# Optimization experiments

Hardware: AMD Instinct MI355X
Metric: run time of the kernel (lower is better)

Reference implementation:

```python
import jax, jax.numpy as jnp
import numpy as np

B, L, W = 512, 16, 256


def setup_inputs() -> dict:
    key = jax.random.key(0)
    k = jax.random.split(key, 9)
    f32 = jnp.float32
    # spin configuration in {-1, +1}
    x = jax.random.randint(k[0], (B, L, L), 0, 2).astype(f32) * 2.0 - 1.0
    s = 1.0 / np.sqrt(W)
    W_ih = jax.random.normal(k[1], (3 * W, 2), f32) * s      # GRUCell input weights
    W_hh = jax.random.normal(k[2], (3 * W, W), f32) * s      # GRUCell hidden weights
    b_ih = jax.random.normal(k[3], (3 * W,), f32) * s
    b_hh = jax.random.normal(k[4], (3 * W,), f32) * s
    W_fc = jax.random.normal(k[5], (2, W), f32) * s          # fc1
    b_fc = jax.random.normal(k[6], (2,), f32) * s
    W_hcat = jax.random.normal(k[7], (W, 2 * W), f32) * (1.0 / np.sqrt(2 * W))  # intermediate_h
    W_xcat = jax.random.normal(k[8], (1, 2), f32) * 0.5      # intermediate_x
    return dict(x=x, W_ih=W_ih, W_hh=W_hh, b_ih=b_ih, b_hh=b_hh,
                W_fc=W_fc, b_fc=b_fc, W_hcat=W_hcat, W_xcat=W_xcat)


def _log_prob(x, W_ih, W_hh, b_ih, b_hh, W_fc, b_fc, W_hcat, W_xcat):
    Bsz, Ln, _ = x.shape
    Wd = W_hh.shape[1]
    mask = (1.0 + x) * 0.5                      # (1+x)/2
    Wh_l = W_hcat[:, :Wd]                       # acts on left-neighbor hidden (cat order: [left, up])
    Wh_u = W_hcat[:, Wd:]                       # acts on up-neighbor hidden

    def step(carry, xs):
        x_left, h_left = carry                  # [B], [B,W]
        x_cur, x_up, h_up, m = xs               # [B], [B], [B,W], [B]
        # intermediate_x(stack([x_left, x_up]))
        x_int = x_left * W_xcat[0, 0] + x_up * W_xcat[0, 1]
        # intermediate_h(cat([h_left, h_up]))
        h_int = h_left @ Wh_l.T + h_up @ Wh_u.T
        # embedded_x = [(x+1)/2, 1-(x+1)/2]
        p_up = (x_int + 1.0) * 0.5
        emb = jnp.stack([p_up, 1.0 - p_up], axis=1)   # [B,2]
        # torch.nn.GRUCell math (gate order: reset, update, new)
        gi = emb @ W_ih.T + b_ih
        gh = h_int @ W_hh.T + b_hh
        ir, iz, inn = jnp.split(gi, 3, axis=1)
        hr, hz, hn = jnp.split(gh, 3, axis=1)
        r = jax.nn.sigmoid(ir + hr)
        z = jax.nn.sigmoid(iz + hz)
        n = jnp.tanh(inn + r * hn)
        h_next = (1.0 - z) * n + z * h_int
        y = jax.nn.log_softmax(h_next @ W_fc.T + b_fc, axis=1)   # [B,2]
        lp = y[:, 0] * m + y[:, 1] * (1.0 - m)
        return (x_cur, h_next), (h_next, lp)

    h_prev = jnp.zeros((Ln, Bsz, Wd), x.dtype)  # hidden of row above, columns-major [L,B,W]
    x_prev = jnp.zeros((Ln, Bsz), x.dtype)      # spins of row above [L,B]
    lp_rows = []
    for i in range(Ln):                         # fixed small structural loop over rows
        x_row = x[:, i, :].T                    # [L,B]
        m_row = mask[:, i, :].T
        x_up, h_up = x_prev, h_prev
        if i % 2 == 1:                          # zigzag: odd rows scan right-to-left
            x_row, m_row = x_row[::-1], m_row[::-1]
            x_up, h_up = x_up[::-1], h_up[::-1]
        carry0 = (jnp.zeros((Bsz,), x.dtype), jnp.zeros((Bsz, Wd), x.dtype))
        _, (h_out, lp_out) = jax.lax.scan(step, carry0, (x_row, x_up, h_up, m_row))
        if i % 2 == 1:                          # restore grid (column) order
            h_out, lp_out = h_out[::-1], lp_out[::-1]
        lp_rows.append(lp_out)                  # [L,B]
        h_prev = h_out
        x_prev = x[:, i, :].T
    lp = jnp.transpose(jnp.stack(lp_rows, axis=0), (2, 0, 1))   # [B,L,L]
    lp = lp.at[:, 0, 0].set(1.0 - mask[:, 0, 0])                # first site overwrite
    return lp.sum(axis=(1, 2))


def reference(x, W_ih, W_hh, b_ih, b_hh, W_fc, b_fc, W_hcat, W_xcat):
    # z2 == 0 and reverse == False: log_prob(x) == _log_prob(x)
    return _log_prob(x, W_ih, W_hh, b_ih, b_hh, W_fc, b_fc, W_hcat, W_xcat)
```

## Files before the change

kernel.cpp:

```cpp
#include <hip/hip_runtime.h>
#include <math.h>

#define LL 16
#define WD 256
#define G3 768

#define OFF_A8  0
#define OFF_B8  32768
#define OFF_SRB 81920
#define OFF_SRA 82688
#define OFF_GA  82944
#define OFF_GBI 83712

__device__ __forceinline__ int sdot4(unsigned a, unsigned b, int acc) {
#if __has_builtin(__builtin_amdgcn_sdot4)
    return __builtin_amdgcn_sdot4((int)a, (int)b, acc, false);
#else
    int s = acc;
    #pragma unroll
    for (int r = 0; r < 4; ++r)
        s += (int)(signed char)(a >> (8 * r)) * (int)(signed char)(b >> (8 * r));
    return s;
#endif
}
__device__ __forceinline__ float fsig(float v) { return 1.f / (1.f + __expf(-v)); }
__device__ __forceinline__ float ftanh_(float v) {
    v = fminf(fmaxf(v, -15.f), 15.f);
    float e = __expf(-2.f * v);
    return (1.f - e) / (1.f + e);
}
__device__ __forceinline__ int clampi8(int q) {
    return q > 127 ? 127 : (q < -127 ? -127 : q);
}

__global__ __launch_bounds__(64)
void gru2d_prep1(const float* __restrict__ W_hh, const float* __restrict__ W_hcat,
                 float* __restrict__ ws) {
    int row = blockIdx.x, lane = threadIdx.x;
    float s = 0.f;
    if (row < 768) {
        for (int k = lane; k < 256; k += 64) s = fmaxf(s, fabsf(W_hh[row * 256 + k]));
    } else {
        int r = row - 768;
        for (int k = lane; k < 512; k += 64) s = fmaxf(s, fabsf(W_hcat[r * 512 + k]));
    }
    #pragma unroll
    for (int o = 32; o > 0; o >>= 1) s = fmaxf(s, __shfl_down(s, o));
    if (lane == 0) {
        float sc = (s > 0.f) ? s * (1.f / 127.f) : 1.f;
        if (row < 768) ws[OFF_SRB + row] = sc;
        else           ws[OFF_SRA + (row - 768)] = sc;
    }
}

__global__ __launch_bounds__(256)
void gru2d_prep2(const float* __restrict__ W_ih, const float* __restrict__ W_hh,
                 const float* __restrict__ b_ih, const float* __restrict__ W_hcat,
                 float* __restrict__ ws) {
    unsigned* __restrict__ wsu = (unsigned*)ws;
    int m = blockIdx.x * 256 + threadIdx.x;
    if (m < 32768) {
        int g4 = m >> 11, t = (m >> 2) & 511, r = m & 3;
        int j = g4 * 4 + r;
        int v = t >> 6, l = t & 63;
        int w = v * 32 + (l & 31), kh = l >> 5;
        float inv = 1.f / ws[OFF_SRA + w];
        int base = w * 512 + kh * 256 + 4 * j;
        unsigned pk = 0;
        #pragma unroll
        for (int bb = 0; bb < 4; ++bb) {
            int qv = clampi8(__float2int_rn(W_hcat[base + bb] * inv));
            pk |= ((unsigned)(qv & 255)) << (8 * bb);
        }
        wsu[OFF_A8 + m] = pk;
    } else if (m < 81920) {
        int mm = m - 32768;
        int g4 = mm >> 11, t = (mm >> 2) & 511, rr = mm & 3;
        int ql = g4 * 4 + rr;
        int gate = ql >> 5, q = ql & 31;
        int v = t >> 6, l = t & 63;
        int w = v * 32 + (l & 31), kh = l >> 5;
        int row = gate * 256 + w;
        float inv = 1.f / ws[OFF_SRB + row];
        int kb = row * 256 + kh * 128 + 4 * q;
        unsigned pk = 0;
        #pragma unroll
        for (int bb = 0; bb < 4; ++bb) {
            int qv = clampi8(__float2int_rn(W_hh[kb + bb] * inv));
            pk |= ((unsigned)(qv & 255)) << (8 * bb);
        }
        wsu[OFF_B8 + mm] = pk;
    } else if (m < 82688) {
        int e = m - 81920;
        float w0 = W_ih[2 * e], w1 = W_ih[2 * e + 1];
        ws[OFF_GA + e] = w0 - w1;
        ws[OFF_GBI + e] = w1 + b_ih[e];
    }
}

__global__ __launch_bounds__(512, 2)
void gru2d_main(const float* __restrict__ x, const float* __restrict__ b_hh,
                const float* __restrict__ W_fc, const float* __restrict__ b_fc,
                const float* __restrict__ W_xcat, const float* __restrict__ ws,
                float* __restrict__ out) {
    __shared__ __attribute__((aligned(16))) unsigned h8[2][64];
    __shared__ __attribute__((aligned(16))) unsigned hp8[2][LL][64];
    __shared__ float hs8[2][8];
    __shared__ float hps8[2][LL][8];
    __shared__ __attribute__((aligned(16))) unsigned hint8q[2][64];
    __shared__ float dqs[2][8];
    __shared__ float fcp[2][2][8];
    __shared__ float sx[2][256];

    const int tid = threadIdx.x;
    const int v = tid >> 6, l = tid & 63;
    const int lr = l & 31, sub = l >> 5;
    const int w = (v << 5) + lr;
    const int b0 = blockIdx.x * 2;
    const unsigned* __restrict__ wsu = (const unsigned*)ws;

    unsigned wA8[64], wB8[96];
    #pragma unroll
    for (int g = 0; g < 16; ++g) {
        uint4 q = ((const uint4*)(wsu + OFF_A8))[g * 512 + tid];
        wA8[4*g] = q.x; wA8[4*g+1] = q.y; wA8[4*g+2] = q.z; wA8[4*g+3] = q.w;
    }
    #pragma unroll
    for (int g = 0; g < 24; ++g) {
        uint4 q = ((const uint4*)(wsu + OFF_B8))[g * 512 + tid];
        wB8[4*g] = q.x; wB8[4*g+1] = q.y; wB8[4*g+2] = q.z; wB8[4*g+3] = q.w;
    }

    const float ascale = ws[OFF_SRA + w];
    float bA[3], bBi[3], bbh[3], bsr[3];
    #pragma unroll
    for (int g = 0; g < 3; ++g) {
        bA[g]  = ws[OFF_GA + (g << 8) + w];
        bBi[g] = ws[OFF_GBI + (g << 8) + w];
        bbh[g] = b_hh[(g << 8) + w];
        bsr[g] = ws[OFF_SRB + (g << 8) + w];
    }
    const float wfc0 = W_fc[w], wfc1 = W_fc[256 + w];
    sx[tid >> 8][tid & 255] = x[(b0 + (tid >> 8)) * 256 + (tid & 255)];
    {
        unsigned* hp = (unsigned*)hp8;
        #pragma unroll
        for (int g = 0; g < 4; ++g) hp[g * 512 + tid] = 0u;
        if (tid < 256) ((float*)hps8)[tid] = 0.f;
    }
    const float xc0 = W_xcat[0], xc1 = W_xcat[1];
    const float bf0 = b_fc[0], bf1 = b_fc[1];
    float lp_acc = 0.f;
    __syncthreads();

    for (int i = 0; i < LL; ++i) {
        const int odd = i & 1;
        const int dir = odd ? -1 : 1;
        const int c0g = odd ? (LL - 1) : 0;
        for (int t = 0; t < LL; ++t) {
            const int col = c0g + dir * t;
            const int sidx = (i << 4) + t;

            #pragma unroll
            for (int g = 0; g < 16; ++g)
                asm volatile("" : "+v"(wA8[4*g]), "+v"(wA8[4*g+1]), "+v"(wA8[4*g+2]), "+v"(wA8[4*g+3]));
            #pragma unroll
            for (int g = 0; g < 24; ++g)
                asm volatile("" : "+v"(wB8[4*g]), "+v"(wB8[4*g+1]), "+v"(wB8[4*g+2]), "+v"(wB8[4*g+3]));

            if ((tid == 0 || tid == 256) && sidx > 0) {
                const int b = tid >> 8;
                int ps = sidx - 1, pi2 = ps >> 4, pt2 = ps & 15;
                int pcol = (pi2 & 1) ? (15 - pt2) : pt2;
                float l0 = bf0, l1 = bf1;
                #pragma unroll
                for (int vv = 0; vv < 8; ++vv) { l0 += fcp[b][0][vv]; l1 += fcp[b][1][vv]; }
                float mx = fmaxf(l0, l1);
                float lse = mx + logf(__expf(l0 - mx) + __expf(l1 - mx));
                float xcur = sx[b][(pi2 << 4) + pcol];
                float mm = (1.f + xcur) * 0.5f;
                float lp = (l0 - lse) * mm + (l1 - lse) * (1.f - mm);
                if (pi2 == 0 && pcol == 0) lp = 1.f - mm;
                lp_acc += lp;
            }

            float hi_sel;
            {
                float fa0 = 0.f, fa1 = 0.f;
                if (!(sub == 0 && t == 0)) {
                    const uint4* H0 = sub ? (const uint4*)hp8[0][col] : (const uint4*)h8[0];
                    const uint4* H1 = sub ? (const uint4*)hp8[1][col] : (const uint4*)h8[1];
                    const float* s0p = sub ? hps8[0][col] : hs8[0];
                    const float* s1p = sub ? hps8[1][col] : hs8[1];
                    #pragma unroll
                    for (int c = 0; c < 8; ++c) {
                        uint4 ua0 = H0[2*c], ub0 = H0[2*c+1];
                        uint4 ua1 = H1[2*c], ub1 = H1[2*c+1];
                        const int kk = c << 3;
                        int a0 = 0, a1 = 0;
                        a0 = sdot4(wA8[kk],   ua0.x, a0); a0 = sdot4(wA8[kk+1], ua0.y, a0);
                        a0 = sdot4(wA8[kk+2], ua0.z, a0); a0 = sdot4(wA8[kk+3], ua0.w, a0);
                        a0 = sdot4(wA8[kk+4], ub0.x, a0); a0 = sdot4(wA8[kk+5], ub0.y, a0);
                        a0 = sdot4(wA8[kk+6], ub0.z, a0); a0 = sdot4(wA8[kk+7], ub0.w, a0);
                        a1 = sdot4(wA8[kk],   ua1.x, a1); a1 = sdot4(wA8[kk+1], ua1.y, a1);
                        a1 = sdot4(wA8[kk+2], ua1.z, a1); a1 = sdot4(wA8[kk+3], ua1.w, a1);
                        a1 = sdot4(wA8[kk+4], ub1.x, a1); a1 = sdot4(wA8[kk+5], ub1.y, a1);
                        a1 = sdot4(wA8[kk+6], ub1.z, a1); a1 = sdot4(wA8[kk+7], ub1.w, a1);
                        fa0 += (float)a0 * s0p[c];
                        fa1 += (float)a1 * s1p[c];
                    }
                    fa0 *= ascale;
                    fa1 *= ascale;
                }
                fa0 += __shfl_xor(fa0, 32);
                fa1 += __shfl_xor(fa1, 32);
                hi_sel = sub ? fa1 : fa0;
                float am = fabsf(hi_sel);
                #pragma unroll
                for (int o = 1; o < 32; o <<= 1) am = fmaxf(am, __shfl_xor(am, o));
                float qsc = 127.f / fmaxf(am, 1e-20f);
                int q = clampi8(__float2int_rn(hi_sel * qsc));
                ((unsigned char*)hint8q)[(sub << 8) + w] = (unsigned char)(q & 255);
                if (lr == 0) dqs[sub][v] = am * (1.f / 127.f);
            }
            __syncthreads();

            {
                const uint4* hq0 = ((const uint4*)hint8q) + (sub << 3);
                const uint4* hq1 = ((const uint4*)hint8q) + 16 + (sub << 3);
                const float* dq0 = &dqs[0][sub << 2];
                const float* dq1 = &dqs[1][sub << 2];
                float gr0 = 0.f, gz0 = 0.f, gn0 = 0.f, gr1 = 0.f, gz1 = 0.f, gn1 = 0.f;
                #pragma unroll
                for (int c2 = 0; c2 < 4; ++c2) {
                    uint4 u0a = hq0[2*c2], u0b = hq0[2*c2+1];
                    uint4 u1a = hq1[2*c2], u1b = hq1[2*c2+1];
                    const int k = c2 << 3;
                    int r0 = 0, z0 = 0, n0 = 0, r1 = 0, z1 = 0, n1 = 0;
                    r0 = sdot4(wB8[k],      u0a.x, r0); r0 = sdot4(wB8[k+1],    u0a.y, r0);
                    r0 = sdot4(wB8[k+2],    u0a.z, r0); r0 = sdot4(wB8[k+3],    u0a.w, r0);
                    r0 = sdot4(wB8[k+4],    u0b.x, r0); r0 = sdot4(wB8[k+5],    u0b.y, r0);
                    r0 = sdot4(wB8[k+6],    u0b.z, r0); r0 = sdot4(wB8[k+7],    u0b.w, r0);
                    z0 = sdot4(wB8[32+k],   u0a.x, z0); z0 = sdot4(wB8[32+k+1], u0a.y, z0);
                    z0 = sdot4(wB8[32+k+2], u0a.z, z0); z0 = sdot4(wB8[32+k+3], u0a.w, z0);
                    z0 = sdot4(wB8[32+k+4], u0b.x, z0); z0 = sdot4(wB8[32+k+5], u0b.y, z0);
                    z0 = sdot4(wB8[32+k+6], u0b.z, z0); z0 = sdot4(wB8[32+k+7], u0b.w, z0);
                    n0 = sdot4(wB8[64+k],   u0a.x, n0); n0 = sdot4(wB8[64+k+1], u0a.y, n0);
                    n0 = sdot4(wB8[64+k+2], u0a.z, n0); n0 = sdot4(wB8[64+k+3], u0a.w, n0);
                    n0 = sdot4(wB8[64+k+4], u0b.x, n0); n0 = sdot4(wB8[64+k+5], u0b.y, n0);
                    n0 = sdot4(wB8[64+k+6], u0b.z, n0); n0 = sdot4(wB8[64+k+7], u0b.w, n0);
                    r1 = sdot4(wB8[k],      u1a.x, r1); r1 = sdot4(wB8[k+1],    u1a.y, r1);
                    r1 = sdot4(wB8[k+2],    u1a.z, r1); r1 = sdot4(wB8[k+3],    u1a.w, r1);
                    r1 = sdot4(wB8[k+4],    u1b.x, r1); r1 = sdot4(wB8[k+5],    u1b.y, r1);
                    r1 = sdot4(wB8[k+6],    u1b.z, r1); r1 = sdot4(wB8[k+7],    u1b.w, r1);
                    z1 = sdot4(wB8[32+k],   u1a.x, z1); z1 = sdot4(wB8[32+k+1], u1a.y, z1);
                    z1 = sdot4(wB8[32+k+2], u1a.z, z1); z1 = sdot4(wB8[32+k+3], u1a.w, z1);
                    z1 = sdot4(wB8[32+k+4], u1b.x, z1); z1 = sdot4(wB8[32+k+5], u1b.y, z1);
                    z1 = sdot4(wB8[32+k+6], u1b.z, z1); z1 = sdot4(wB8[32+k+7], u1b.w, z1);
                    n1 = sdot4(wB8[64+k],   u1a.x, n1); n1 = sdot4(wB8[64+k+1], u1a.y, n1);
                    n1 = sdot4(wB8[64+k+2], u1a.z, n1); n1 = sdot4(wB8[64+k+3], u1a.w, n1);
                    n1 = sdot4(wB8[64+k+4], u1b.x, n1); n1 = sdot4(wB8[64+k+5], u1b.y, n1);
                    n1 = sdot4(wB8[64+k+6], u1b.z, n1); n1 = sdot4(wB8[64+k+7], u1b.w, n1);
                    const float d0 = dq0[c2], d1 = dq1[c2];
                    gr0 += (float)r0 * d0; gz0 += (float)z0 * d0; gn0 += (float)n0 * d0;
                    gr1 += (float)r1 * d1; gz1 += (float)z1 * d1; gn1 += (float)n1 * d1;
                }
                gr0 += __shfl_xor(gr0, 32); gz0 += __shfl_xor(gz0, 32); gn0 += __shfl_xor(gn0, 32);
                gr1 += __shfl_xor(gr1, 32); gz1 += __shfl_xor(gz1, 32); gn1 += __shfl_xor(gn1, 32);

                const int bsel = sub;
                float GR = (bsel ? gr1 : gr0) * bsr[0];
                float GZ = (bsel ? gz1 : gz0) * bsr[1];
                float GN = (bsel ? gn1 : gn0) * bsr[2];
                float xl = (t == 0) ? 0.f : sx[bsel][(i << 4) + col - dir];
                float xu = (i == 0) ? 0.f : sx[bsel][((i - 1) << 4) + col];
                float pu = (xl * xc0 + xu * xc1 + 1.f) * 0.5f;
                float rr_ = fsig(bA[0] * pu + bBi[0] + GR + bbh[0]);
                float zz = fsig(bA[1] * pu + bBi[1] + GZ + bbh[1]);
                float nn = ftanh_(bA[2] * pu + bBi[2] + rr_ * (GN + bbh[2]));
                float hn = (1.f - zz) * nn + zz * hi_sel;

                float am = fabsf(hn);
                #pragma unroll
                for (int o = 1; o < 32; o <<= 1) am = fmaxf(am, __shfl_xor(am, o));
                float qs = 127.f / fmaxf(am, 1e-20f);
                int q = clampi8(__float2int_rn(hn * qs));
                ((unsigned char*)h8)[(sub << 8) + w] = (unsigned char)(q & 255);
                ((unsigned char*)hp8)[(sub << 12) + (col << 8) + w] = (unsigned char)(q & 255);
                if (lr == 0) {
                    float hsc = am * (1.f / 127.f);
                    hs8[sub][v] = hsc;
                    hps8[sub][col][v] = hsc;
                }

                float s0 = hn * wfc0, s1 = hn * wfc1;
                #pragma unroll
                for (int o = 1; o < 32; o <<= 1) {
                    s0 += __shfl_xor(s0, o);
                    s1 += __shfl_xor(s1, o);
                }
                if (lr == 0) { fcp[sub][0][v] = s0; fcp[sub][1][v] = s1; }
            }
            __syncthreads();
        }
    }

    if (tid == 0 || tid == 256) {
        const int b = tid >> 8;
        float l0 = bf0, l1 = bf1;
        #pragma unroll
        for (int vv = 0; vv < 8; ++vv) { l0 += fcp[b][0][vv]; l1 += fcp[b][1][vv]; }
        float mx = fmaxf(l0, l1);
        float lse = mx + logf(__expf(l0 - mx) + __expf(l1 - mx));
        float xcur = sx[b][15 * 16 + 0];
        float mm = (1.f + xcur) * 0.5f;
        lp_acc += (l0 - lse) * mm + (l1 - lse) * (1.f - mm);
        out[b0 + b] = lp_acc;
    }
}

extern "C" void kernel_launch(void* const* d_in, const int* in_sizes, int n_in,
                              void* d_out, int out_size, void* d_ws, size_t ws_size,
                              hipStream_t stream) {
    const float* x      = (const float*)d_in[0];
    const float* W_ih   = (const float*)d_in[1];
    const float* W_hh   = (const float*)d_in[2];
    const float* b_ih   = (const float*)d_in[3];
    const float* b_hh   = (const float*)d_in[4];
    const float* W_fc   = (const float*)d_in[5];
    const float* b_fc   = (const float*)d_in[6];
    const float* W_hcat = (const float*)d_in[7];
    const float* W_xcat = (const float*)d_in[8];
    float* out = (float*)d_out;
    float* ws  = (float*)d_ws;

    gru2d_prep1<<<1024, 64, 0, stream>>>(W_hh, W_hcat, ws);
    gru2d_prep2<<<323, 256, 0, stream>>>(W_ih, W_hh, b_ih, W_hcat, ws);
    gru2d_main<<<256, 512, 0, stream>>>(x, b_hh, W_fc, b_fc, W_xcat, ws, out);
}
```

Baseline: 899.4 us.

## Repartition W_hcat int8 matvec across quarter-waves and use DPP reductions

The prep kernel re-packs the W_hcat int8 weights so that each lane covers two output rows over a quarter of the K dimension, in place of one row over half of K. The hidden-state and scale loads are halved per lane and scales are fetched as float4. Cross-lane max and sum reductions for quantization and fc1 now use DPP row permutes within 16 lanes plus a single shuffle, instead of five-step shuffle loops. The aim is to cut LDS traffic and cross-lane shuffle latency on the serial recurrence path. The cost is more partial accumulators and extra shuffles to combine the K-quarters.

```diff
diff --git a/kernel.cpp b/kernel.cpp
--- a/kernel.cpp
+++ b/kernel.cpp
@@ -31,6 +31,26 @@
 }
 __device__ __forceinline__ int clampi8(int q) {
     return q > 127 ? 127 : (q < -127 ? -127 : q);
+}
+
+template <int CTRL>
+__device__ __forceinline__ float dppf(float x) {
+    return __builtin_bit_cast(float, __builtin_amdgcn_update_dpp(
+        0, __builtin_bit_cast(int, x), CTRL, 0xF, 0xF, true));
+}
+__device__ __forceinline__ float max16(float x) {
+    x = fmaxf(x, dppf<0xB1>(x));
+    x = fmaxf(x, dppf<0x4E>(x));
+    x = fmaxf(x, dppf<0x124>(x));
+    x = fmaxf(x, dppf<0x128>(x));
+    return x;
+}
+__device__ __forceinline__ float sum16(float x) {
+    x += dppf<0xB1>(x);
+    x += dppf<0x4E>(x);
+    x += dppf<0x124>(x);
+    x += dppf<0x128>(x);
+    return x;
 }
 
 __global__ __launch_bounds__(64)
@@ -60,12 +80,14 @@
     unsigned* __restrict__ wsu = (unsigned*)ws;
     int m = blockIdx.x * 256 + threadIdx.x;
     if (m < 32768) {
-        int g4 = m >> 11, t = (m >> 2) & 511, r = m & 3;
-        int j = g4 * 4 + r;
-        int v = t >> 6, l = t & 63;
-        int w = v * 32 + (l & 31), kh = l >> 5;
-        float inv = 1.f / ws[OFF_SRA + w];
-        int base = w * 512 + kh * 256 + 4 * j;
+        int g = m >> 11, t = (m >> 2) & 511, r = m & 3;
+        int jj = g * 4 + r;
+        int v = t >> 6, l = t & 63, lr = l & 31, sub = l >> 5, q2 = lr >> 4;
+        int row = (v << 5) + (lr & 15) + ((jj >> 5) << 4);
+        int j = jj & 31;
+        int qk = (sub << 1) | q2;
+        float inv = 1.f / ws[OFF_SRA + row];
+        int base = row * 512 + (qk << 7) + 4 * j;
         unsigned pk = 0;
         #pragma unroll
         for (int bb = 0; bb < 4; ++bb) {
@@ -105,17 +127,19 @@
                 float* __restrict__ out) {
     __shared__ __attribute__((aligned(16))) unsigned h8[2][64];
     __shared__ __attribute__((aligned(16))) unsigned hp8[2][LL][64];
-    __shared__ float hs8[2][8];
-    __shared__ float hps8[2][LL][8];
+    __shared__ __attribute__((aligned(16))) float hs8[2][8];
+    __shared__ __attribute__((aligned(16))) float hps8[2][LL][8];
     __shared__ __attribute__((aligned(16))) unsigned hint8q[2][64];
-    __shared__ float dqs[2][8];
+    __shared__ __attribute__((aligned(16))) float dqs[2][8];
     __shared__ float fcp[2][2][8];
     __shared__ float sx[2][256];
 
     const int tid = threadIdx.x;
     const int v = tid >> 6, l = tid & 63;
     const int lr = l & 31, sub = l >> 5;
+    const int q2 = lr >> 4;
     const int w = (v << 5) + lr;
+    const int rA0 = (v << 5) + (lr & 15);
     const int b0 = blockIdx.x * 2;
     const unsigned* __restrict__ wsu = (const unsigned*)ws;
 
@@ -131,7 +155,8 @@
         wB8[4*g] = q.x; wB8[4*g+1] = q.y; wB8[4*g+2] = q.z; wB8[4*g+3] = q.w;
     }
 
-    const float ascale = ws[OFF_SRA + w];
+    const float asc0 = ws[OFF_SRA + rA0];
+    const float asc1 = ws[OFF_SRA + rA0 + 16];
     float bA[3], bBi[3], bbh[3], bsr[3];
     #pragma unroll
     for (int g = 0; g < 3; ++g) {
@@ -186,50 +211,75 @@
 
             float hi_sel;
             {
-                float fa0 = 0.f, fa1 = 0.f;
+                float f00 = 0.f, f01 = 0.f, f10 = 0.f, f11 = 0.f;
                 if (!(sub == 0 && t == 0)) {
-                    const uint4* H0 = sub ? (const uint4*)hp8[0][col] : (const uint4*)h8[0];
-                    const uint4* H1 = sub ? (const uint4*)hp8[1][col] : (const uint4*)h8[1];
-                    const float* s0p = sub ? hps8[0][col] : hs8[0];
-                    const float* s1p = sub ? hps8[1][col] : hs8[1];
+                    const uint4* H0;
+                    const uint4* H1;
+                    const float4* S0;
+                    const float4* S1;
+                    if (sub == 0) {
+                        H0 = ((const uint4*)h8[0]) + (q2 << 3);
+                        H1 = ((const uint4*)h8[1]) + (q2 << 3);
+                        S0 = ((const float4*)hs8[0]) + q2;
+                        S1 = ((const float4*)hs8[1]) + q2;
+                    } else {
+                        H0 = ((const uint4*)hp8[0][col]) + (q2 << 3);
+                        H1 = ((const uint4*)hp8[1][col]) + (q2 << 3);
+                        S0 = ((const float4*)hps8[0][col]) + q2;
+                        S1 = ((const float4*)hps8[1][col]) + q2;
+                    }
+                    const float4 sc0 = *S0, sc1 = *S1;
                     #pragma unroll
-                    for (int c = 0; c < 8; ++c) {
+                    for (int c = 0; c < 4; ++c) {
                         uint4 ua0 = H0[2*c], ub0 = H0[2*c+1];
                         uint4 ua1 = H1[2*c], ub1 = H1[2*c+1];
-                        const int kk = c << 3;
-                        int a0 = 0, a1 = 0;
-                        a0 = sdot4(wA8[kk],   ua0.x, a0); a0 = sdot4(wA8[kk+1], ua0.y, a0);
-                        a0 = sdot4(wA8[kk+2], ua0.z, a0); a0 = sdot4(wA8[kk+3], ua0.w, a0);
-                        a0 = sdot4(wA8[kk+4], ub0.x, a0); a0 = sdot4(wA8[kk+5], ub0.y, a0);
-                        a0 = sdot4(wA8[kk+6], ub0.z, a0); a0 = sdot4(wA8[kk+7], ub0.w, a0);
-                        a1 = sdot4(wA8[kk],   ua1.x, a1); a1 = sdot4(wA8[kk+1], ua1.y, a1);
-                        a1 = sdot4(wA8[kk+2], ua1.z, a1); a1 = sdot4(wA8[kk+3], ua1.w, a1);
-                        a1 = sdot4(wA8[kk+4], ub1.x, a1); a1 = sdot4(wA8[kk+5], ub1.y, a1);
-                        a1 = sdot4(wA8[kk+6], ub1.z, a1); a1 = sdot4(wA8[kk+7], ub1.w, a1);
-                        fa0 += (float)a0 * s0p[c];
-                        fa1 += (float)a1 * s1p[c];
+                        const int e = c << 3;
+                        int a00 = 0, a01 = 0, a10 = 0, a11 = 0;
+                        a00 = sdot4(wA8[e],   ua0.x, a00); a00 = sdot4(wA8[e+1], ua0.y, a00);
+                        a00 = sdot4(wA8[e+2], ua0.z, a00); a00 = sdot4(wA8[e+3], ua0.w, a00);
+                        a00 = sdot4(wA8[e+4], ub0.x, a00); a00 = sdot4(wA8[e+5], ub0.y, a00);
+                        a00 = sdot4(wA8[e+6], ub0.z, a00); a00 = sdot4(wA8[e+7], ub0.w, a00);
+                        a10 = sdot4(wA8[32+e],   ua0.x, a10); a10 = sdot4(wA8[32+e+1], ua0.y, a10);
+                        a10 = sdot4(wA8[32+e+2], ua0.z, a10); a10 = sdot4(wA8[32+e+3], ua0.w, a10);
+                        a10 = sdot4(wA8[32+e+4], ub0.x, a10); a10 = sdot4(wA8[32+e+5], ub0.y, a10);
+                        a10 = sdot4(wA8[32+e+6], ub0.z, a10); a10 = sdot4(wA8[32+e+7], ub0.w, a10);
+                        a01 = sdot4(wA8[e],   ua1.x, a01); a01 = sdot4(wA8[e+1], ua1.y, a01);
+                        a01 = sdot4(wA8[e+2], ua1.z, a01); a01 = sdot4(wA8[e+3], ua1.w, a01);
+                        a01 = sdot4(wA8[e+4], ub1.x, a01); a01 = sdot4(wA8[e+5], ub1.y, a01);
+                        a01 = sdot4(wA8[e+6], ub1.z, a01); a01 = sdot4(wA8[e+7], ub1.w, a01);
+                        a11 = sdot4(wA8[32+e],   ua1.x, a11); a11 = sdot4(wA8[32+e+1], ua1.y, a11);
+                        a11 = sdot4(wA8[32+e+2], ua1.z, a11); a11 = sdot4(wA8[32+e+3], ua1.w, a11);
+                        a11 = sdot4(wA8[32+e+4], ub1.x, a11); a11 = sdot4(wA8[32+e+5], ub1.y, a11);
+                        a11 = sdot4(wA8[32+e+6], ub1.z, a11); a11 = sdot4(wA8[32+e+7], ub1.w, a11);
+                        const float s0c = ((const float*)&sc0)[c];
+                        const float s1c = ((const float*)&sc1)[c];
+                        f00 += (float)a00 * s0c; f01 += (float)a01 * s1c;
+                        f10 += (float)a10 * s0c; f11 += (float)a11 * s1c;
                     }
-                    fa0 *= ascale;
-                    fa1 *= ascale;
+                    f00 *= asc0; f01 *= asc0;
+                    f10 *= asc1; f11 *= asc1;
                 }
-                fa0 += __shfl_xor(fa0, 32);
-                fa1 += __shfl_xor(fa1, 32);
-                hi_sel = sub ? fa1 : fa0;
-                float am = fabsf(hi_sel);
-                #pragma unroll
-                for (int o = 1; o < 32; o <<= 1) am = fmaxf(am, __shfl_xor(am, o));
-                float qsc = 127.f / fmaxf(am, 1e-20f);
+                f00 += __shfl_xor(f00, 16); f00 += __shfl_xor(f00, 32);
+                f01 += __shfl_xor(f01, 16); f01 += __shfl_xor(f01, 32);
+                f10 += __shfl_xor(f10, 16); f10 += __shfl_xor(f10, 32);
+                f11 += __shfl_xor(f11, 16); f11 += __shfl_xor(f11, 32);
+
+                hi_sel = q2 ? (sub ? f11 : f10) : (sub ? f01 : f00);
+
+                float m_ = fmaxf(fabsf(sub ? f01 : f00), fabsf(sub ? f11 : f10));
+                m_ = max16(m_);
+                float qsc = 127.f / fmaxf(m_, 1e-20f);
                 int q = clampi8(__float2int_rn(hi_sel * qsc));
                 ((unsigned char*)hint8q)[(sub << 8) + w] = (unsigned char)(q & 255);
-                if (lr == 0) dqs[sub][v] = am * (1.f / 127.f);
+                if (lr == 0) dqs[sub][v] = m_ * (1.f / 127.f);
             }
             __syncthreads();
 
             {
                 const uint4* hq0 = ((const uint4*)hint8q) + (sub << 3);
                 const uint4* hq1 = ((const uint4*)hint8q) + 16 + (sub << 3);
-                const float* dq0 = &dqs[0][sub << 2];
-                const float* dq1 = &dqs[1][sub << 2];
+                const float4 dq0v = ((const float4*)dqs[0])[sub];
+                const float4 dq1v = ((const float4*)dqs[1])[sub];
                 float gr0 = 0.f, gz0 = 0.f, gn0 = 0.f, gr1 = 0.f, gz1 = 0.f, gn1 = 0.f;
                 #pragma unroll
                 for (int c2 = 0; c2 < 4; ++c2) {
@@ -261,7 +311,8 @@
                     n1 = sdot4(wB8[64+k+2], u1a.z, n1); n1 = sdot4(wB8[64+k+3], u1a.w, n1);
                     n1 = sdot4(wB8[64+k+4], u1b.x, n1); n1 = sdot4(wB8[64+k+5], u1b.y, n1);
                     n1 = sdot4(wB8[64+k+6], u1b.z, n1); n1 = sdot4(wB8[64+k+7], u1b.w, n1);
-                    const float d0 = dq0[c2], d1 = dq1[c2];
+                    const float d0 = ((const float*)&dq0v)[c2];
+                    const float d1 = ((const float*)&dq1v)[c2];
                     gr0 += (float)r0 * d0; gz0 += (float)z0 * d0; gn0 += (float)n0 * d0;
                     gr1 += (float)r1 * d1; gz1 += (float)z1 * d1; gn1 += (float)n1 * d1;
                 }
@@ -280,9 +331,8 @@
                 float nn = ftanh_(bA[2] * pu + bBi[2] + rr_ * (GN + bbh[2]));
                 float hn = (1.f - zz) * nn + zz * hi_sel;
 
-                float am = fabsf(hn);
-                #pragma unroll
-                for (int o = 1; o < 32; o <<= 1) am = fmaxf(am, __shfl_xor(am, o));
+                float am = max16(fabsf(hn));
+                am = fmaxf(am, __shfl_xor(am, 16));
                 float qs = 127.f / fmaxf(am, 1e-20f);
                 int q = clampi8(__float2int_rn(hn * qs));
                 ((unsigned char*)h8)[(sub << 8) + w] = (unsigned char)(q & 255);
@@ -294,11 +344,8 @@
                 }
 
                 float s0 = hn * wfc0, s1 = hn * wfc1;
-                #pragma unroll
-                for (int o = 1; o < 32; o <<= 1) {
-                    s0 += __shfl_xor(s0, o);
-                    s1 += __shfl_xor(s1, o);
-                }
+                s0 = sum16(s0); s0 += __shfl_xor(s0, 16);
+                s1 = sum16(s1); s1 += __shfl_xor(s1, 16);
                 if (lr == 0) { fcp[sub][0][v] = s0; fcp[sub][1][v] = s1; }
             }
             __syncthreads();
```

After: 785.7 us. -12.6%, faster.
